# Kernel optimization log

Measured on AMD Instinct MI355X. Metric: run time of the kernel, lower is better.

## Reference

```python
import jax, jax.numpy as jnp
import numpy as np
from math import sqrt

ALPHA = 1.0
EPS = 1e-8


def setup_inputs() -> dict:
    key = jax.random.key(0)
    k1, k2, k3 = jax.random.split(key, 3)
    B, L, S, H, E = 4, 2048, 2048, 16, 64
    queries = jax.random.normal(k1, (B, L, H, E), dtype=jnp.float32)
    keys = jax.random.normal(k2, (B, S, H, E), dtype=jnp.float32)
    values = jax.random.normal(k3, (B, S, H, E), dtype=jnp.float32)
    return {"queries": queries, "keys": keys, "values": values}


def reference(queries, keys, values):
    B, L, H, E = queries.shape
    scale = 1.0 / sqrt(E)
    # dot product scores: [B,H,L,S]
    dot = jnp.einsum('blhe,bshe->bhls', queries, keys)
    # squared norms: [B,H,L,1] and [B,H,1,S]
    qn2 = jnp.sum(queries * queries, axis=-1).transpose(0, 2, 1)[..., :, None]
    kn2 = jnp.sum(keys * keys, axis=-1).transpose(0, 2, 1)[..., None, :]
    # wedge (parallelogram area) norm^2 = |q|^2|k|^2 - (q.k)^2, clipped at 0
    wedge_norm = jnp.sqrt(jax.nn.relu(qn2 * kn2 - dot * dot) + EPS)
    scores = ((1.0 - ALPHA) * dot + ALPHA * wedge_norm) * scale
    A = jax.nn.softmax(scores, axis=-1)  # no mask (mask_flag=False), dropout=0
    V = jnp.einsum('bhls,bshd->blhd', A, values)
    return V, jnp.mean(jnp.abs(scores))
```

## Files before the change

### kernel.cpp

```cpp
#include <hip/hip_runtime.h>
#include <math.h>

constexpr int Bb = 4, Ll = 2048, Ss = 2048, Hh = 16, Ee = 64;
constexpr float S2E  = 0.125f * 1.44269504088896341f;
constexpr float EPS2 = 1e-8f * S2E * S2E;
constexpr float INV_CNT = 1.0f / (4.0f * 16.0f * 2048.0f * 2048.0f);
constexpr float SUM_SCALE = INV_CNT * 0.69314718055994531f;

typedef __attribute__((ext_vector_type(8)))  short short8;
typedef __attribute__((ext_vector_type(4)))  float floatx4;
typedef __attribute__((ext_vector_type(16))) float floatx16;

#define MFMA32 __builtin_amdgcn_mfma_f32_32x32x16_bf16

#define GLL(gp, lp_)                                                       \
  __builtin_amdgcn_global_load_lds(                                        \
      (const __attribute__((address_space(1))) unsigned int*)(gp),         \
      (__attribute__((address_space(3))) unsigned int*)(lp_), 16, 0, 0)

__device__ __forceinline__ unsigned bfrnd(float f) {
  unsigned u = __builtin_bit_cast(unsigned, f);
  return u + 0x7fffu + ((u >> 16) & 1u);
}
__device__ __forceinline__ float sq4(float4 v) {
  return v.x * v.x + v.y * v.y + v.z * v.z + v.w * v.w;
}
__device__ __forceinline__ float4 mul4(float4 v, float s) {
  float4 r; r.x = v.x * s; r.y = v.y * s; r.z = v.z * s; r.w = v.w * s;
  return r;
}
__device__ __forceinline__ short8 pack8(float4 x, float4 y) {
  union { short8 s; unsigned u[4]; } r;
  r.u[0] = __builtin_amdgcn_perm(bfrnd(x.y), bfrnd(x.x), 0x07060302u);
  r.u[1] = __builtin_amdgcn_perm(bfrnd(x.w), bfrnd(x.z), 0x07060302u);
  r.u[2] = __builtin_amdgcn_perm(bfrnd(y.y), bfrnd(y.x), 0x07060302u);
  r.u[3] = __builtin_amdgcn_perm(bfrnd(y.w), bfrnd(y.z), 0x07060302u);
  return r.s;
}
__device__ __forceinline__ void pl32swap(unsigned &a, unsigned &b) {
  asm("v_permlane32_swap_b32 %0, %1" : "+v"(a), "+v"(b));
}

__global__ __launch_bounds__(256) void geom_pre_kernel(
    const float* __restrict__ Kg, const float* __restrict__ Vg,
    short* __restrict__ Kbf, short* __restrict__ Vtg,
    float* __restrict__ kn2g, float* __restrict__ sumg) {
  __shared__ __align__(16) short vsm[64 * 66];
  const int tid = threadIdx.x, bid = blockIdx.x;
  const int st = bid & 31, h = (bid >> 5) & 15, b = bid >> 9;
  const int s0 = st * 64, bh = b * 16 + h;
  if (bid == 0 && tid == 0) *sumg = 0.0f;

  const int r64 = tid >> 2, ec = (tid & 3) * 16;
  const float4* kp = (const float4*)(Kg + (((size_t)b * Ss + s0 + r64) * Hh + h) * Ee + ec);
  float4 k0 = kp[0], k1 = kp[1], k2 = kp[2], k3 = kp[3];
  float kn = sq4(k0) + sq4(k1) + sq4(k2) + sq4(k3);
  kn += __shfl_xor(kn, 1);
  kn += __shfl_xor(kn, 2);
  if ((tid & 3) == 0) kn2g[(size_t)bh * Ss + s0 + r64] = kn;
  short* ko = Kbf + ((size_t)bh * Ss + s0 + r64) * Ee + ec;
  *(short8*)(ko)     = pack8(k0, k1);
  *(short8*)(ko + 8) = pack8(k2, k3);

  const int sq = tid >> 4, eq = tid & 15;
  const float* vb = Vg + (((size_t)b * Ss + s0 + sq * 4) * Hh + h) * Ee + eq * 4;
  float4 r0 = *(const float4*)(vb);
  float4 r1 = *(const float4*)(vb + Hh * Ee);
  float4 r2 = *(const float4*)(vb + 2 * Hh * Ee);
  float4 r3 = *(const float4*)(vb + 3 * Hh * Ee);
#pragma unroll
  for (int j = 0; j < 4; ++j) {
    unsigned lo = __builtin_amdgcn_perm(bfrnd((&r1.x)[j]), bfrnd((&r0.x)[j]), 0x07060302u);
    unsigned hh = __builtin_amdgcn_perm(bfrnd((&r3.x)[j]), bfrnd((&r2.x)[j]), 0x07060302u);
    short* row = vsm + (eq * 4 + j) * 66 + sq * 4;
    *(unsigned*)(row)     = lo;
    *(unsigned*)(row + 2) = hh;
  }
  __syncthreads();
  const int e = tid >> 2, sc = (tid & 3) * 16;
  const short* rr = vsm + e * 66 + sc;
  uint4 a, c;
  a.x = *(const unsigned*)(rr + 0);  a.y = *(const unsigned*)(rr + 2);
  a.z = *(const unsigned*)(rr + 4);  a.w = *(const unsigned*)(rr + 6);
  c.x = *(const unsigned*)(rr + 8);  c.y = *(const unsigned*)(rr + 10);
  c.z = *(const unsigned*)(rr + 12); c.w = *(const unsigned*)(rr + 14);
  short* vo = Vtg + ((size_t)bh * Ee + e) * Ss + s0 + sc;
  *(uint4*)(vo)     = a;
  *(uint4*)(vo + 8) = c;
}

constexpr int KB0 = 0, VB0 = 12288, KN2 = 24576;

__global__ __launch_bounds__(256, 4) void geom_attn_kernel(
    const float* __restrict__ Qg, const short* __restrict__ Kbf,
    const short* __restrict__ Vtg, const float* __restrict__ kn2g,
    float* __restrict__ outg, float* __restrict__ sumg) {
  __shared__ __align__(16) char smem[32768];

  const int tid = threadIdx.x, w = tid >> 6, lane = tid & 63;
  const int l31 = lane & 31, hi = lane >> 5;
  const int bid = blockIdx.x;
  const int wk = ((bid & 7) << 7) | (bid >> 3);
  const int lt = wk & 15, h = (wk >> 4) & 15, b = wk >> 8;
  const int bh = b * 16 + h;
  const int l0w = lt * 128 + w * 32;

  short8 qB[4];
  float qn2v;
  {
    const float* qrow = Qg + (((size_t)b * Ll + l0w + l31) * Hh + h) * Ee;
    float qn = 0.f;
#pragma unroll
    for (int ks = 0; ks < 4; ++ks) {
      float4 a0 = mul4(*(const float4*)(qrow + ks * 16 + hi * 8), S2E);
      float4 a1 = mul4(*(const float4*)(qrow + ks * 16 + hi * 8 + 4), S2E);
      qn += sq4(a0) + sq4(a1);
      qB[ks] = pack8(a0, a1);
    }
    qn += __shfl_xor(qn, 32);
    qn2v = qn;
  }

  const int rK = tid >> 3, pK = tid & 7;
  const char* kSrc = (const char*)Kbf + (size_t)bh * (Ss * 128) + rK * 128 + ((pK ^ (rK & 7)) * 16);
  const int eV = tid >> 2;
  const char* vSrc = (const char*)Vtg + (size_t)bh * (Ss * 128) + eV * (Ss * 2) + (((tid & 3) ^ (eV & 3)) * 16);
  char* kDstW = smem + KB0 + w * 1024;
  char* vDstW = smem + VB0 + w * 1024;

  {
    const char* knSrc = (const char*)kn2g + (size_t)bh * 8192 + (size_t)tid * 16;
    GLL(knSrc, smem + KN2 + w * 1024);
    GLL(knSrc + 4096, smem + KN2 + w * 1024 + 4096);
  }

  GLL(kSrc, kDstW);
  GLL(vSrc, vDstW);
  kSrc += 4096; vSrc += 64;
  GLL(kSrc, kDstW + 4096);
  GLL(vSrc, vDstW + 4096);
  kSrc += 4096; vSrc += 64;

  floatx16 o[2] = {};
  float lp = 0.f, scsum = 0.f;

  const int kSwz = l31 & 7;
  const int vSwz = l31 & 3;

  int pb = 0;
  for (int it = 0; it < 64; ++it) {
    if (it == 63) asm volatile("s_waitcnt vmcnt(0)" ::: "memory");
    else          asm volatile("s_waitcnt vmcnt(2)" ::: "memory");
    __builtin_amdgcn_s_barrier();
    asm volatile("" ::: "memory");

    if (it < 62) {
      const int pf = pb ? pb - 1 : 2;
      GLL(kSrc, kDstW + pf * 4096);
      GLL(vSrc, vDstW + pf * 4096);
      kSrc += 4096; vSrc += 64;
    }

    const char* Kb = smem + KB0 + pb * 4096;
    const char* Vb = smem + VB0 + pb * 4096;

    short8 ka0 = *(const short8*)(Kb + l31 * 128 + (((0 + hi) ^ kSwz) * 16));
    short8 ka1 = *(const short8*)(Kb + l31 * 128 + (((2 + hi) ^ kSwz) * 16));
    short8 ka2 = *(const short8*)(Kb + l31 * 128 + (((4 + hi) ^ kSwz) * 16));
    short8 ka3 = *(const short8*)(Kb + l31 * 128 + (((6 + hi) ^ kSwz) * 16));
    __builtin_amdgcn_s_setprio(1);
    floatx16 d = {};
    d = MFMA32(ka0, qB[0], d, 0, 0, 0);
    d = MFMA32(ka1, qB[1], d, 0, 0, 0);
    d = MFMA32(ka2, qB[2], d, 0, 0, 0);
    d = MFMA32(ka3, qB[3], d, 0, 0, 0);
    __builtin_amdgcn_s_setprio(0);

    short8 vb00 = *(const short8*)(Vb + l31 * 64 + (((0 + hi) ^ vSwz) * 16));
    short8 vb01 = *(const short8*)(Vb + l31 * 64 + (((2 + hi) ^ vSwz) * 16));
    short8 vb10 = *(const short8*)(Vb + (32 + l31) * 64 + (((0 + hi) ^ vSwz) * 16));
    short8 vb11 = *(const short8*)(Vb + (32 + l31) * 64 + (((2 + hi) ^ vSwz) * 16));

    float4 knv0 = *(const float4*)(smem + KN2 + it * 128 + 0 * 32 + hi * 16);
    float4 knv1 = *(const float4*)(smem + KN2 + it * 128 + 1 * 32 + hi * 16);
    float4 knv2 = *(const float4*)(smem + KN2 + it * 128 + 2 * 32 + hi * 16);
    float4 knv3 = *(const float4*)(smem + KN2 + it * 128 + 3 * 32 + hi * 16);

    unsigned pk[4][2];
#pragma unroll
    for (int q = 0; q < 4; ++q) {
      const float4 knq = (q == 0) ? knv0 : (q == 1) ? knv1 : (q == 2) ? knv2 : knv3;
      float pe[4], rt4[4];
#pragma unroll
      for (int r = 0; r < 4; ++r) {
        float dot = d[4 * q + r];
        float w2 = fmaf(-dot, dot, qn2v * (&knq.x)[r]);
        w2 = fmaxf(w2, EPS2);
        rt4[r] = __builtin_amdgcn_sqrtf(w2);
        pe[r]  = __builtin_amdgcn_exp2f(rt4[r]);
      }
      scsum += (rt4[0] + rt4[1]) + (rt4[2] + rt4[3]);
      lp    += (pe[0] + pe[1]) + (pe[2] + pe[3]);
      pk[q][0] = __builtin_amdgcn_perm(__builtin_bit_cast(unsigned, pe[1]),
                                       __builtin_bit_cast(unsigned, pe[0]), 0x07060302u);
      pk[q][1] = __builtin_amdgcn_perm(__builtin_bit_cast(unsigned, pe[3]),
                                       __builtin_bit_cast(unsigned, pe[2]), 0x07060302u);
    }

    pl32swap(pk[0][0], pk[1][0]);
    pl32swap(pk[0][1], pk[1][1]);
    pl32swap(pk[2][0], pk[3][0]);
    pl32swap(pk[2][1], pk[3][1]);
    union { unsigned u[4]; short8 s; } pa0, pa1;
    pa0.u[0] = pk[0][0]; pa0.u[1] = pk[0][1]; pa0.u[2] = pk[1][0]; pa0.u[3] = pk[1][1];
    pa1.u[0] = pk[2][0]; pa1.u[1] = pk[2][1]; pa1.u[2] = pk[3][0]; pa1.u[3] = pk[3][1];

    __builtin_amdgcn_s_setprio(1);
    o[0] = MFMA32(pa0.s, vb00, o[0], 0, 0, 0);
    o[0] = MFMA32(pa1.s, vb01, o[0], 0, 0, 0);
    o[1] = MFMA32(pa0.s, vb10, o[1], 0, 0, 0);
    o[1] = MFMA32(pa1.s, vb11, o[1], 0, 0, 0);
    __builtin_amdgcn_s_setprio(0);

    pb = (pb == 2) ? 0 : pb + 1;
  }

  __syncthreads();

  lp += __shfl_xor(lp, 32);
  float lpinv = 1.0f / lp;

#pragma unroll
  for (int r = 0; r < 16; ++r) {
    const int row = (r & 3) + 8 * (r >> 2) + 4 * hi;
    float inv = __shfl(lpinv, row);
    float* orow = outg + (((size_t)b * Ll + l0w + row) * Hh + h) * Ee + l31;
    orow[0]  = o[0][r] * inv;
    orow[32] = o[1][r] * inv;
  }

  scsum += __shfl_xor(scsum, 1);
  scsum += __shfl_xor(scsum, 2);
  scsum += __shfl_xor(scsum, 4);
  scsum += __shfl_xor(scsum, 8);
  scsum += __shfl_xor(scsum, 16);
  scsum += __shfl_xor(scsum, 32);
  if (lane == 0) atomicAdd(sumg, scsum * SUM_SCALE);
}

extern "C" void kernel_launch(void* const* d_in, const int* in_sizes, int n_in,
                              void* d_out, int out_size, void* d_ws, size_t ws_size,
                              hipStream_t stream) {
  const float* Q = (const float*)d_in[0];
  const float* K = (const float*)d_in[1];
  const float* V = (const float*)d_in[2];
  float* out   = (float*)d_out;
  float* sumsc = out + (size_t)Bb * Ll * Hh * Ee;

  short* Kbf = (short*)d_ws;
  short* Vtg = Kbf + (size_t)Bb * Hh * Ss * Ee;
  float* kn2 = (float*)(Vtg + (size_t)Bb * Hh * Ee * Ss);

  hipLaunchKernelGGL(geom_pre_kernel, dim3(Bb * Hh * (Ss / 64)), dim3(256), 0,
                     stream, K, V, Kbf, Vtg, kn2, sumsc);
  hipLaunchKernelGGL(geom_attn_kernel, dim3(Bb * Hh * (Ll / 128)), dim3(256), 0,
                     stream, Q, Kbf, Vtg, kn2, out, sumsc);
}
```

Before: 253.3 us.

## Process 64-key tiles with double buffering instead of 32-key triple buffering

The main loop now handles 64 keys per iteration in two 32-key halves, using a double-buffered LDS pipeline of 8 KB K and V tiles in place of the earlier triple-buffered 4 KB tiles. This halves the number of barriers and waitcnt points and gives the scheduler two independent QK MFMA chains to interleave with the softmax math. V rows become 128 bytes with an 8-way swizzle, matching the K layout. In exchange, LDS grows to 40 KB per block, each wait drains all outstanding loads (vmcnt(0)), and prefetch depth drops from two tiles ahead to one.

```diff
diff --git a/kernel.cpp b/kernel.cpp
--- a/kernel.cpp
+++ b/kernel.cpp
@@ -89,13 +89,13 @@
   *(uint4*)(vo + 8) = c;
 }
 
-constexpr int KB0 = 0, VB0 = 12288, KN2 = 24576;
+constexpr int KB0 = 0, VB0 = 16384, KN2 = 32768;
 
 __global__ __launch_bounds__(256, 4) void geom_attn_kernel(
     const float* __restrict__ Qg, const short* __restrict__ Kbf,
     const short* __restrict__ Vtg, const float* __restrict__ kn2g,
     float* __restrict__ outg, float* __restrict__ sumg) {
-  __shared__ __align__(16) char smem[32768];
+  __shared__ __align__(16) char smem[40960];
 
   const int tid = threadIdx.x, w = tid >> 6, lane = tid & 63;
   const int l31 = lane & 31, hi = lane >> 5;
@@ -122,9 +122,10 @@
   }
 
   const int rK = tid >> 3, pK = tid & 7;
-  const char* kSrc = (const char*)Kbf + (size_t)bh * (Ss * 128) + rK * 128 + ((pK ^ (rK & 7)) * 16);
-  const int eV = tid >> 2;
-  const char* vSrc = (const char*)Vtg + (size_t)bh * (Ss * 128) + eV * (Ss * 2) + (((tid & 3) ^ (eV & 3)) * 16);
+  const char* kSrc = (const char*)Kbf + (size_t)bh * (Ss * 128)
+                     + rK * 128 + ((pK ^ (rK & 7)) * 16);
+  const char* vSrc = (const char*)Vtg + (size_t)bh * (Ss * 128)
+                     + rK * (Ss * 2) + ((pK ^ (rK & 7)) * 16);
   char* kDstW = smem + KB0 + w * 1024;
   char* vDstW = smem + VB0 + w * 1024;
 
@@ -133,67 +134,27 @@
     GLL(knSrc, smem + KN2 + w * 1024);
     GLL(knSrc + 4096, smem + KN2 + w * 1024 + 4096);
   }
-
   GLL(kSrc, kDstW);
+  GLL(kSrc + 4096, kDstW + 4096);
   GLL(vSrc, vDstW);
-  kSrc += 4096; vSrc += 64;
-  GLL(kSrc, kDstW + 4096);
-  GLL(vSrc, vDstW + 4096);
-  kSrc += 4096; vSrc += 64;
+  GLL(vSrc + 32 * (Ss * 2), vDstW + 4096);
+  kSrc += 8192; vSrc += 128;
 
   floatx16 o[2] = {};
   float lp = 0.f, scsum = 0.f;
 
   const int kSwz = l31 & 7;
-  const int vSwz = l31 & 3;
-
-  int pb = 0;
-  for (int it = 0; it < 64; ++it) {
-    if (it == 63) asm volatile("s_waitcnt vmcnt(0)" ::: "memory");
-    else          asm volatile("s_waitcnt vmcnt(2)" ::: "memory");
-    __builtin_amdgcn_s_barrier();
-    asm volatile("" ::: "memory");
-
-    if (it < 62) {
-      const int pf = pb ? pb - 1 : 2;
-      GLL(kSrc, kDstW + pf * 4096);
-      GLL(vSrc, vDstW + pf * 4096);
-      kSrc += 4096; vSrc += 64;
-    }
-
-    const char* Kb = smem + KB0 + pb * 4096;
-    const char* Vb = smem + VB0 + pb * 4096;
-
-    short8 ka0 = *(const short8*)(Kb + l31 * 128 + (((0 + hi) ^ kSwz) * 16));
-    short8 ka1 = *(const short8*)(Kb + l31 * 128 + (((2 + hi) ^ kSwz) * 16));
-    short8 ka2 = *(const short8*)(Kb + l31 * 128 + (((4 + hi) ^ kSwz) * 16));
-    short8 ka3 = *(const short8*)(Kb + l31 * 128 + (((6 + hi) ^ kSwz) * 16));
-    __builtin_amdgcn_s_setprio(1);
-    floatx16 d = {};
-    d = MFMA32(ka0, qB[0], d, 0, 0, 0);
-    d = MFMA32(ka1, qB[1], d, 0, 0, 0);
-    d = MFMA32(ka2, qB[2], d, 0, 0, 0);
-    d = MFMA32(ka3, qB[3], d, 0, 0, 0);
-    __builtin_amdgcn_s_setprio(0);
-
-    short8 vb00 = *(const short8*)(Vb + l31 * 64 + (((0 + hi) ^ vSwz) * 16));
-    short8 vb01 = *(const short8*)(Vb + l31 * 64 + (((2 + hi) ^ vSwz) * 16));
-    short8 vb10 = *(const short8*)(Vb + (32 + l31) * 64 + (((0 + hi) ^ vSwz) * 16));
-    short8 vb11 = *(const short8*)(Vb + (32 + l31) * 64 + (((2 + hi) ^ vSwz) * 16));
-
-    float4 knv0 = *(const float4*)(smem + KN2 + it * 128 + 0 * 32 + hi * 16);
-    float4 knv1 = *(const float4*)(smem + KN2 + it * 128 + 1 * 32 + hi * 16);
-    float4 knv2 = *(const float4*)(smem + KN2 + it * 128 + 2 * 32 + hi * 16);
-    float4 knv3 = *(const float4*)(smem + KN2 + it * 128 + 3 * 32 + hi * 16);
-
+  const int vSwz = l31 & 7;
+
+  auto sm = [&](const floatx16& dd, int knByte, short8& paA, short8& paB) {
     unsigned pk[4][2];
 #pragma unroll
     for (int q = 0; q < 4; ++q) {
-      const float4 knq = (q == 0) ? knv0 : (q == 1) ? knv1 : (q == 2) ? knv2 : knv3;
+      float4 knq = *(const float4*)(smem + knByte + q * 32 + hi * 16);
       float pe[4], rt4[4];
 #pragma unroll
       for (int r = 0; r < 4; ++r) {
-        float dot = d[4 * q + r];
+        float dot = dd[4 * q + r];
         float w2 = fmaf(-dot, dot, qn2v * (&knq.x)[r]);
         w2 = fmaxf(w2, EPS2);
         rt4[r] = __builtin_amdgcn_sqrtf(w2);
@@ -206,26 +167,90 @@
       pk[q][1] = __builtin_amdgcn_perm(__builtin_bit_cast(unsigned, pe[3]),
                                        __builtin_bit_cast(unsigned, pe[2]), 0x07060302u);
     }
-
     pl32swap(pk[0][0], pk[1][0]);
     pl32swap(pk[0][1], pk[1][1]);
     pl32swap(pk[2][0], pk[3][0]);
     pl32swap(pk[2][1], pk[3][1]);
-    union { unsigned u[4]; short8 s; } pa0, pa1;
-    pa0.u[0] = pk[0][0]; pa0.u[1] = pk[0][1]; pa0.u[2] = pk[1][0]; pa0.u[3] = pk[1][1];
-    pa1.u[0] = pk[2][0]; pa1.u[1] = pk[2][1]; pa1.u[2] = pk[3][0]; pa1.u[3] = pk[3][1];
-
-    __builtin_amdgcn_s_setprio(1);
-    o[0] = MFMA32(pa0.s, vb00, o[0], 0, 0, 0);
-    o[0] = MFMA32(pa1.s, vb01, o[0], 0, 0, 0);
-    o[1] = MFMA32(pa0.s, vb10, o[1], 0, 0, 0);
-    o[1] = MFMA32(pa1.s, vb11, o[1], 0, 0, 0);
-    __builtin_amdgcn_s_setprio(0);
-
-    pb = (pb == 2) ? 0 : pb + 1;
-  }
-
-  __syncthreads();
+    union { unsigned u[4]; short8 s; } A, B;
+    A.u[0] = pk[0][0]; A.u[1] = pk[0][1]; A.u[2] = pk[1][0]; A.u[3] = pk[1][1];
+    B.u[0] = pk[2][0]; B.u[1] = pk[2][1]; B.u[2] = pk[3][0]; B.u[3] = pk[3][1];
+    paA = A.s; paB = B.s;
+  };
+
+  asm volatile("s_waitcnt vmcnt(0)" ::: "memory");
+  __builtin_amdgcn_s_barrier();
+  asm volatile("" ::: "memory");
+
+  for (int it = 0; it < 32; ++it) {
+    const int p = it & 1;
+    if (it) {
+      asm volatile("s_waitcnt vmcnt(0)" ::: "memory");
+      __builtin_amdgcn_s_barrier();
+      asm volatile("" ::: "memory");
+    }
+    if (it < 31) {
+      const int pn = p ^ 1;
+      GLL(kSrc, kDstW + pn * 8192);
+      GLL(kSrc + 4096, kDstW + pn * 8192 + 4096);
+      GLL(vSrc, vDstW + pn * 8192);
+      GLL(vSrc + 32 * (Ss * 2), vDstW + pn * 8192 + 4096);
+      kSrc += 8192; vSrc += 128;
+    }
+    const char* Kb = smem + KB0 + p * 8192;
+    const char* Vb = smem + VB0 + p * 8192;
+    const int knByte = KN2 + it * 256;
+
+    short8 ka0 = *(const short8*)(Kb + l31 * 128 + (((0 + hi) ^ kSwz) * 16));
+    short8 ka1 = *(const short8*)(Kb + l31 * 128 + (((2 + hi) ^ kSwz) * 16));
+    short8 ka2 = *(const short8*)(Kb + l31 * 128 + (((4 + hi) ^ kSwz) * 16));
+    short8 ka3 = *(const short8*)(Kb + l31 * 128 + (((6 + hi) ^ kSwz) * 16));
+    __builtin_amdgcn_s_setprio(1);
+    floatx16 d0 = {};
+    d0 = MFMA32(ka0, qB[0], d0, 0, 0, 0);
+    d0 = MFMA32(ka1, qB[1], d0, 0, 0, 0);
+    d0 = MFMA32(ka2, qB[2], d0, 0, 0, 0);
+    d0 = MFMA32(ka3, qB[3], d0, 0, 0, 0);
+    __builtin_amdgcn_s_setprio(0);
+
+    short8 kb0 = *(const short8*)(Kb + 4096 + l31 * 128 + (((0 + hi) ^ kSwz) * 16));
+    short8 kb1 = *(const short8*)(Kb + 4096 + l31 * 128 + (((2 + hi) ^ kSwz) * 16));
+    short8 kb2 = *(const short8*)(Kb + 4096 + l31 * 128 + (((4 + hi) ^ kSwz) * 16));
+    short8 kb3 = *(const short8*)(Kb + 4096 + l31 * 128 + (((6 + hi) ^ kSwz) * 16));
+    __builtin_amdgcn_s_setprio(1);
+    floatx16 d1 = {};
+    d1 = MFMA32(kb0, qB[0], d1, 0, 0, 0);
+    d1 = MFMA32(kb1, qB[1], d1, 0, 0, 0);
+    d1 = MFMA32(kb2, qB[2], d1, 0, 0, 0);
+    d1 = MFMA32(kb3, qB[3], d1, 0, 0, 0);
+    __builtin_amdgcn_s_setprio(0);
+
+    short8 paA, paB;
+    sm(d0, knByte, paA, paB);
+
+    short8 vb00 = *(const short8*)(Vb + l31 * 128 + (((0 + hi) ^ vSwz) * 16));
+    short8 vb01 = *(const short8*)(Vb + l31 * 128 + (((2 + hi) ^ vSwz) * 16));
+    short8 vb10 = *(const short8*)(Vb + (32 + l31) * 128 + (((0 + hi) ^ vSwz) * 16));
+    short8 vb11 = *(const short8*)(Vb + (32 + l31) * 128 + (((2 + hi) ^ vSwz) * 16));
+    __builtin_amdgcn_s_setprio(1);
+    o[0] = MFMA32(paA, vb00, o[0], 0, 0, 0);
+    o[0] = MFMA32(paB, vb01, o[0], 0, 0, 0);
+    o[1] = MFMA32(paA, vb10, o[1], 0, 0, 0);
+    o[1] = MFMA32(paB, vb11, o[1], 0, 0, 0);
+    __builtin_amdgcn_s_setprio(0);
+
+    sm(d1, knByte + 128, paA, paB);
+
+    vb00 = *(const short8*)(Vb + l31 * 128 + (((4 + hi) ^ vSwz) * 16));
+    vb01 = *(const short8*)(Vb + l31 * 128 + (((6 + hi) ^ vSwz) * 16));
+    vb10 = *(const short8*)(Vb + (32 + l31) * 128 + (((4 + hi) ^ vSwz) * 16));
+    vb11 = *(const short8*)(Vb + (32 + l31) * 128 + (((6 + hi) ^ vSwz) * 16));
+    __builtin_amdgcn_s_setprio(1);
+    o[0] = MFMA32(paA, vb00, o[0], 0, 0, 0);
+    o[0] = MFMA32(paB, vb01, o[0], 0, 0, 0);
+    o[1] = MFMA32(paA, vb10, o[1], 0, 0, 0);
+    o[1] = MFMA32(paB, vb11, o[1], 0, 0, 0);
+    __builtin_amdgcn_s_setprio(0);
+  }
 
   lp += __shfl_xor(lp, 32);
   float lpinv = 1.0f / lp;
```

Result: slower. 282.4 us (+11.5%).
